# Optimization experiments

Measured on AMD Instinct MI355X. Metric: run time of the kernel, lower is better.

The kernel has to match this reference:

```python
import jax, jax.numpy as jnp
import numpy as np

B, CIN, COUT, H, W = 4, 4, 8, 256, 256
FFTH, FFTW = 2 * H - 1, 2 * W - 1  # fftsize = insize + outsize - 1 (padding=True, stride=1)


def setup_inputs() -> dict:
    key = jax.random.key(0)
    k_im, k_w, k_b = jax.random.split(key, 3)
    im = jax.random.normal(k_im, (B, CIN, H, W), dtype=jnp.float32)
    # learned frequency-domain kernel, last dim = (real, imag)
    weight = jax.random.normal(k_w, (COUT, CIN, FFTH, FFTW, 2), dtype=jnp.float32)
    bias = jax.random.normal(k_b, (COUT, 1, 1), dtype=jnp.float32)
    return {"im": im, "weight": weight, "bias": bias}


def reference(im, weight, bias):
    b, cin, h, w = im.shape
    ffth, fftw = 2 * h - 1, 2 * w - 1
    # zero-pad spatially to fftsize; imaginary part is zero (torch pads a trailing complex dim)
    im_p = jnp.pad(im, ((0, 0), (0, 0), (0, ffth - h), (0, fftw - w)))
    f_im = jnp.fft.fft2(im_p.astype(jnp.complex64))              # [B, Cin, fftH, fftW]
    wc = jax.lax.complex(weight[..., 0], weight[..., 1])         # [O, Cin, fftH, fftW]
    # broadcast complex multiply + in-channel reduction fused as a per-frequency contraction;
    # ifft is linear so summing over in-channels before ifft matches the original math
    feats = jnp.einsum('bchw,ochw->bohw', f_im, wc)              # [B, O, fftH, fftW]
    real = jnp.fft.ifft2(feats).real                             # real_feats_mode='index' -> real part
    # crop: cropsize = fftsize - insize = (H-1, W-1); left = floor/2, right = ceil/2
    cl_h, cr_h = (h - 1) // 2, h // 2
    cl_w, cr_w = (w - 1) // 2, w // 2
    real = real[:, :, cl_h:ffth - cr_h, cl_w:fftw - cr_w]        # [B, O, H, W]
    return real + bias                                           # bias [O,1,1] broadcasts
```

## Files before the change

kernel.cpp:

```cpp
#include <hip/hip_runtime.h>
#include <math.h>

#define NN 511
#define HH 256
#define BB 4
#define CINC 4
#define COUTC 8
#define CROP 127
#define INV_NN2 (1.0f / ((float)NN * (float)NN))

typedef _Float16 f16;
typedef _Float16 f16x2 __attribute__((ext_vector_type(2)));
typedef _Float16 f16x8 __attribute__((ext_vector_type(8)));
typedef float    f32x4 __attribute__((ext_vector_type(4)));

__device__ __forceinline__ void twid(int a, int b, float& c, float& s) {
    int m = (a * b) % NN;
    float phi = (float)(2.0 * M_PI / (double)NN) * (float)m;
    __sincosf(phi, &s, &c);
}

__global__ void prep_all(const float* __restrict__ im,
                         f16* __restrict__ Aa, f16* __restrict__ Bb,
                         f16* __restrict__ Bd, f16* __restrict__ Ae,
                         f16* __restrict__ imT) {
    int idx = blockIdx.x * 256 + threadIdx.x;
    if (idx < 131072) {
        int m = idx >> 8, y = idx & 255;
        float c, s;
        if (m < 256) { twid(m, y, c, s);       Aa[idx] = (f16)c;    }
        else         { twid(m - 256, y, c, s); Aa[idx] = (f16)(-s); }
    } else if (idx < 655360) {
        int i = idx - 131072;
        int n = i >> 9, k = i & 511;
        int v = n >> 1, ri = n & 1;
        float val = 0.f;
        if (v < NN) {
            int x = k & 255;
            float c, s; twid(v, x, c, s);
            if (ri == 0) val = (k < 256) ? c  : s;
            else         val = (k < 256) ? -s : c;
        }
        Bb[i] = (f16)val;
    } else if (idx < 1179648) {
        int i = idx - 655360;
        int n = i >> 10, k = i & 1023;
        int v = k >> 1, ri = k & 1;
        float val = 0.f;
        if (v < NN) {
            int x = n & 255;
            float c, s; twid(v, x + CROP, c, s);
            if (ri == 0) val = (n < 256) ? c  : s;
            else         val = (n < 256) ? -s : c;
        }
        Bd[i] = (f16)val;
    } else if (idx < 1310720) {
        int i = idx - 1179648;
        int y = i >> 9, k = i & 511;
        float c, s;
        if (k < 256) { twid(k, y + CROP, c, s);       Ae[i] = (f16)c;    }
        else         { twid(k - 256, y + CROP, c, s); Ae[i] = (f16)(-s); }
    } else if (idx < 2359296) {
        int i = idx - 1310720;
        int bc = i >> 16, r = i & 65535;
        int y = r >> 8, x = r & 255;
        imT[(size_t)bc * 65536 + x * 256 + y] = (f16)im[i];
    }
}

#define GLB_PTR(p) ((const __attribute__((address_space(1))) unsigned int*)(p))
#define LDS_PTR(p) ((__attribute__((address_space(3))) unsigned int*)(p))
__device__ __forceinline__ void gld16(const f16* g, f16* l) {
    __builtin_amdgcn_global_load_lds(GLB_PTR(g), LDS_PTR(l), 16, 0, 0);
}

#define STAGE(Abuf, Bbuf)                         \
    do {                                          \
        gld16(Ap,            (Abuf) + o8);        \
        gld16(Ap + 32 * ldA, (Abuf) + o8 + 2048); \
        gld16(Ap + 64 * ldA, (Abuf) + o8 + 4096); \
        gld16(Ap + 96 * ldA, (Abuf) + o8 + 6144); \
        gld16(Bp,            (Bbuf) + o8);        \
        gld16(Bp + 32 * ldB, (Bbuf) + o8 + 2048); \
        Ap += 64; Bp += 64;                       \
    } while (0)

#define COMPUTE(Abuf, Bbuf)                                                   \
    do {                                                                      \
        const f16* a_col = (Abuf) + (wm + col) * 64;                          \
        const f16* b_col = (Bbuf) + (wn + col) * 64;                          \
        f16x8 af[4][2], bf[2][2];                                             \
        _Pragma("unroll")                                                     \
        for (int i = 0; i < 4; ++i) {                                         \
            af[i][0] = *(const f16x8*)(a_col + i * 16 * 64 + offK0);          \
            af[i][1] = *(const f16x8*)(a_col + i * 16 * 64 + offK1);          \
        }                                                                     \
        _Pragma("unroll")                                                     \
        for (int j = 0; j < 2; ++j) {                                         \
            bf[j][0] = *(const f16x8*)(b_col + j * 16 * 64 + offK0);          \
            bf[j][1] = *(const f16x8*)(b_col + j * 16 * 64 + offK1);          \
        }                                                                     \
        _Pragma("unroll")                                                     \
        for (int kk = 0; kk < 2; ++kk)                                        \
            _Pragma("unroll")                                                 \
            for (int i = 0; i < 4; ++i)                                       \
                _Pragma("unroll")                                             \
                for (int j = 0; j < 2; ++j)                                   \
                    acc[i][j] = __builtin_amdgcn_mfma_f32_16x16x32_f16(       \
                        af[i][kk], bf[j][kk], acc[i][j], 0, 0, 0);            \
    } while (0)

#define GEMM_PREAMBLE                                                         \
    const int t    = threadIdx.x;                                             \
    const int row  = t >> 3;                                                  \
    const int slot = t & 7;                                                   \
    const int kg   = (slot ^ (row & 7)) << 3;                                 \
    const f16* Ap = A  + (size_t)(m0 + row) * ldA + kg;                       \
    const f16* Bp = Bt + (size_t)(n0 + row) * ldB + kg;                       \
    const int o8 = t * 8;                                                     \
    const int lane = t & 63, w = t >> 6;                                      \
    const int wm = (w >> 1) * 64, wn = (w & 1) * 32;                          \
    const int col = lane & 15, quad = lane >> 4;                              \
    const int aswz = col & 7;                                                 \
    const int offK0 = ((quad)     ^ aswz) << 3;                               \
    const int offK1 = ((4 + quad) ^ aswz) << 3;                               \
    f32x4 acc[4][2] = {};                                                     \
    STAGE(As0, Bs0);                                                          \
    for (int kb = 0; kb < Kt; kb += 2) {                                      \
        __syncthreads();                                                      \
        STAGE(As1, Bs1);                                                      \
        COMPUTE(As0, Bs0);                                                    \
        __syncthreads();                                                      \
        if (kb + 2 < Kt) STAGE(As0, Bs0);                                     \
        COMPUTE(As1, Bs1);                                                    \
    }

template<int EPI>
__global__ __launch_bounds__(256)
void gemm128x64(const f16* __restrict__ A, const f16* __restrict__ Bt,
                f16* __restrict__ Ch, float* __restrict__ Cf,
                const float* __restrict__ bias,
                int Kt, int ldA, int ldB, size_t sA, size_t sB) {
    __shared__ __align__(16) f16 As0[128 * 64];
    __shared__ __align__(16) f16 As1[128 * 64];
    __shared__ __align__(16) f16 Bs0[64 * 64];
    __shared__ __align__(16) f16 Bs1[64 * 64];

    const int z  = blockIdx.z;
    const int m0 = blockIdx.x * 128;
    const int n0 = blockIdx.y * 64;
    A  += (size_t)z * sA;
    Bt += (size_t)z * sB;

    GEMM_PREAMBLE

    #pragma unroll
    for (int i = 0; i < 4; ++i)
    #pragma unroll
    for (int j = 0; j < 2; ++j) {
        const int mbase = m0 + wm + i * 16 + quad * 4;
        const int ncol  = n0 + wn + j * 16 + col;
        #pragma unroll
        for (int r = 0; r < 4; ++r) {
            const int mm = mbase + r;
            const float val = acc[i][j][r];
            if constexpr (EPI == 0) {
                int u = mm & 255;
                int slotc = (mm < 256) ? ncol : 256 + ncol;
                Ch[((size_t)(u * 16 + z)) * 512 + slotc] = (f16)val;
            } else if constexpr (EPI == 2) {
                int bo = mm >> 8, u = mm & 255;
                int x     = (ncol < 256) ? ncol : ncol - 256;
                int slotc = (ncol < 256) ? u : 256 + u;
                Ch[((size_t)((bo << 8) + x)) * 512 + slotc] = (f16)val;
            } else {
                int bo = ncol >> 8, x = ncol & 255;
                Cf[((size_t)bo * 256 + mm) * 256 + x] = val + bias[bo & 7];
            }
        }
    }
}

#define LSTR 68
__global__ __launch_bounds__(256)
void gemmB_fused(const f16* __restrict__ A, const f16* __restrict__ Bt,
                 const float2* __restrict__ W, f16* __restrict__ feats) {
    __shared__ __align__(16) f16 As0[128 * 64];
    __shared__ __align__(16) f16 As1[128 * 64];
    __shared__ __align__(16) f16 Bs0[64 * 64];
    __shared__ __align__(16) f16 Bs1[64 * 64];

    const int m0 = blockIdx.x * 128;
    const int n0 = blockIdx.y * 64;
    const int Kt = 8, ldA = 512, ldB = 512;

    GEMM_PREAMBLE

    f16* Ls = As0;
    __syncthreads();
    #pragma unroll
    for (int i = 0; i < 4; ++i)
    #pragma unroll
    for (int j = 0; j < 2; ++j) {
        const int ml = wm + i * 16 + quad * 4;
        const int nl = wn + j * 16 + col;
        #pragma unroll
        for (int r = 0; r < 4; ++r)
            Ls[(ml + r) * LSTR + nl] = (f16)acc[i][j][r];
    }
    __syncthreads();

    const int du = t >> 5, dv = t & 31;
    const int u = (m0 >> 4) + du;
    const int v = (n0 >> 1) + dv;
    const int u2 = (u == 0) ? 0 : NN - u;
    const int v2 = (v == 0) ? 0 : NN - v;
    const float gu = (u == 0) ? INV_NN2 : 2.f * INV_NN2;

    float fr[16], fi[16];
    #pragma unroll
    for (int bc = 0; bc < 16; ++bc) {
        f16x2 p = *(const f16x2*)&Ls[(du * 16 + bc) * LSTR + dv * 2];
        fr[bc] = (float)p.x;
        fi[bc] = (float)p.y;
    }

    #pragma unroll
    for (int o = 0; o < COUTC; ++o) {
        float whr[CINC], whi[CINC];
        #pragma unroll
        for (int c = 0; c < CINC; ++c) {
            size_t base = (size_t)(o * CINC + c) * NN;
            float2 w1 = W[(base + u)  * NN + v];
            float2 w2 = W[(base + u2) * NN + v2];
            whr[c] = 0.5f * (w1.x + w2.x);
            whi[c] = 0.5f * (w1.y - w2.y);
        }
        #pragma unroll
        for (int b = 0; b < BB; ++b) {
            float hr = 0.f, hi = 0.f;
            #pragma unroll
            for (int c = 0; c < CINC; ++c) {
                hr += fr[b * 4 + c] * whr[c] - fi[b * 4 + c] * whi[c];
                hi += fr[b * 4 + c] * whi[c] + fi[b * 4 + c] * whr[c];
            }
            f16x2 outp; outp.x = (f16)(hr * gu); outp.y = (f16)(hi * gu);
            *(f16x2*)&feats[((size_t)((b * COUTC + o) * 256 + u)) * 1024 + v * 2] = outp;
        }
    }
}

extern "C" void kernel_launch(void* const* d_in, const int* in_sizes, int n_in,
                              void* d_out, int out_size, void* d_ws, size_t ws_size,
                              hipStream_t stream) {
    const float*  im   = (const float*)d_in[0];
    const float2* W    = (const float2*)d_in[1];
    const float*  bias = (const float*)d_in[2];
    float*        out  = (float*)d_out;

    char* ws = (char*)d_ws;
    f16* Aa    = (f16*)(ws);
    f16* Bb    = (f16*)(ws + 262144);
    f16* Bd    = (f16*)(ws + 1310720);
    f16* Ae    = (f16*)(ws + 2359296);
    f16* imT   = (f16*)(ws + 2621440);
    f16* T1    = (f16*)(ws + 4718592);
    f16* feats = (f16*)(ws + 8912896);
    f16* T2t   = (f16*)(ws + 25690112);

    prep_all<<<9216, 256, 0, stream>>>(im, Aa, Bb, Bd, Ae, imT);

    gemm128x64<0><<<dim3(4, 4, 16), 256, 0, stream>>>(Aa, imT, T1, nullptr, nullptr,
                                                      4, 256, 256, 0, 65536);
    gemmB_fused<<<dim3(32, 16), 256, 0, stream>>>(T1, Bb, W, feats);

    gemm128x64<2><<<dim3(64, 8, 1), 256, 0, stream>>>(feats, Bd, T2t, nullptr, nullptr,
                                                      16, 1024, 1024, 0, 0);
    gemm128x64<3><<<dim3(2, 128, 1), 256, 0, stream>>>(Ae, T2t, nullptr, out, bias,
                                                       8, 512, 512, 0, 0);
}
```

Baseline: 150.3 us.

## Switch GEMM tiles to 32x32x16 MFMA and coalesce image transpose writes

New measurement: 148.5 us. No clear change (-1.2%).

```diff
diff --git a/kernel.cpp b/kernel.cpp
--- a/kernel.cpp
+++ b/kernel.cpp
@@ -12,7 +12,7 @@
 typedef _Float16 f16;
 typedef _Float16 f16x2 __attribute__((ext_vector_type(2)));
 typedef _Float16 f16x8 __attribute__((ext_vector_type(8)));
-typedef float    f32x4 __attribute__((ext_vector_type(4)));
+typedef float    f32x16 __attribute__((ext_vector_type(16)));
 
 __device__ __forceinline__ void twid(int a, int b, float& c, float& s) {
     int m = (a * b) % NN;
@@ -63,8 +63,8 @@
     } else if (idx < 2359296) {
         int i = idx - 1310720;
         int bc = i >> 16, r = i & 65535;
-        int y = r >> 8, x = r & 255;
-        imT[(size_t)bc * 65536 + x * 256 + y] = (f16)im[i];
+        int x = r >> 8, y = r & 255;
+        imT[i] = (f16)im[(size_t)bc * 65536 + y * 256 + x];
     }
 }
 
@@ -87,27 +87,15 @@
 
 #define COMPUTE(Abuf, Bbuf)                                                   \
     do {                                                                      \
-        const f16* a_col = (Abuf) + (wm + col) * 64;                          \
-        const f16* b_col = (Bbuf) + (wn + col) * 64;                          \
-        f16x8 af[4][2], bf[2][2];                                             \
         _Pragma("unroll")                                                     \
-        for (int i = 0; i < 4; ++i) {                                         \
-            af[i][0] = *(const f16x8*)(a_col + i * 16 * 64 + offK0);          \
-            af[i][1] = *(const f16x8*)(a_col + i * 16 * 64 + offK1);          \
+        for (int s = 0; s < 4; ++s) {                                         \
+            const int off = (((s << 1) | kh) ^ swz) << 3;                     \
+            f16x8 a0 = *(const f16x8*)((Abuf) + (wm + ln31) * 64 + off);      \
+            f16x8 a1 = *(const f16x8*)((Abuf) + (wm + 32 + ln31) * 64 + off); \
+            f16x8 b  = *(const f16x8*)((Bbuf) + (wn + ln31) * 64 + off);      \
+            acc0 = __builtin_amdgcn_mfma_f32_32x32x16_f16(a0, b, acc0, 0, 0, 0); \
+            acc1 = __builtin_amdgcn_mfma_f32_32x32x16_f16(a1, b, acc1, 0, 0, 0); \
         }                                                                     \
-        _Pragma("unroll")                                                     \
-        for (int j = 0; j < 2; ++j) {                                         \
-            bf[j][0] = *(const f16x8*)(b_col + j * 16 * 64 + offK0);          \
-            bf[j][1] = *(const f16x8*)(b_col + j * 16 * 64 + offK1);          \
-        }                                                                     \
-        _Pragma("unroll")                                                     \
-        for (int kk = 0; kk < 2; ++kk)                                        \
-            _Pragma("unroll")                                                 \
-            for (int i = 0; i < 4; ++i)                                       \
-                _Pragma("unroll")                                             \
-                for (int j = 0; j < 2; ++j)                                   \
-                    acc[i][j] = __builtin_amdgcn_mfma_f32_16x16x32_f16(       \
-                        af[i][kk], bf[j][kk], acc[i][j], 0, 0, 0);            \
     } while (0)
 
 #define GEMM_PREAMBLE                                                         \
@@ -120,11 +108,9 @@
     const int o8 = t * 8;                                                     \
     const int lane = t & 63, w = t >> 6;                                      \
     const int wm = (w >> 1) * 64, wn = (w & 1) * 32;                          \
-    const int col = lane & 15, quad = lane >> 4;                              \
-    const int aswz = col & 7;                                                 \
-    const int offK0 = ((quad)     ^ aswz) << 3;                               \
-    const int offK1 = ((4 + quad) ^ aswz) << 3;                               \
-    f32x4 acc[4][2] = {};                                                     \
+    const int ln31 = lane & 31, kh = lane >> 5;                               \
+    const int swz = ln31 & 7;                                                 \
+    f32x16 acc0 = {}, acc1 = {};                                              \
     STAGE(As0, Bs0);                                                          \
     for (int kb = 0; kb < Kt; kb += 2) {                                      \
         __syncthreads();                                                      \
@@ -133,6 +119,18 @@
         __syncthreads();                                                      \
         if (kb + 2 < Kt) STAGE(As0, Bs0);                                     \
         COMPUTE(As1, Bs1);                                                    \
+    }
+
+#define EPILOOP(...)                                                          \
+    _Pragma("unroll")                                                         \
+    for (int ib = 0; ib < 2; ++ib) {                                          \
+        _Pragma("unroll")                                                     \
+        for (int r = 0; r < 16; ++r) {                                        \
+            const int ml   = wm + ib * 32 + (r & 3) + 8 * (r >> 2) + 4 * kh;  \
+            const int ncol = n0 + wn + ln31;                                  \
+            const float val = ib ? acc1[r] : acc0[r];                         \
+            __VA_ARGS__                                                       \
+        }                                                                     \
     }
 
 template<int EPI>
@@ -154,31 +152,24 @@
 
     GEMM_PREAMBLE
 
-    #pragma unroll
-    for (int i = 0; i < 4; ++i)
-    #pragma unroll
-    for (int j = 0; j < 2; ++j) {
-        const int mbase = m0 + wm + i * 16 + quad * 4;
-        const int ncol  = n0 + wn + j * 16 + col;
-        #pragma unroll
-        for (int r = 0; r < 4; ++r) {
-            const int mm = mbase + r;
-            const float val = acc[i][j][r];
-            if constexpr (EPI == 0) {
-                int u = mm & 255;
-                int slotc = (mm < 256) ? ncol : 256 + ncol;
-                Ch[((size_t)(u * 16 + z)) * 512 + slotc] = (f16)val;
-            } else if constexpr (EPI == 2) {
-                int bo = mm >> 8, u = mm & 255;
-                int x     = (ncol < 256) ? ncol : ncol - 256;
-                int slotc = (ncol < 256) ? u : 256 + u;
-                Ch[((size_t)((bo << 8) + x)) * 512 + slotc] = (f16)val;
-            } else {
-                int bo = ncol >> 8, x = ncol & 255;
-                Cf[((size_t)bo * 256 + mm) * 256 + x] = val + bias[bo & 7];
-            }
-        }
-    }
+    EPILOOP(
+        const int mm = m0 + ml;
+        if constexpr (EPI == 0) {
+            int u = mm & 255;
+            int slotc = (mm < 256) ? ncol : 256 + ncol;
+            Ch[((size_t)(u * 16 + z)) * 512 + slotc] = (f16)val;
+        } else if constexpr (EPI == 2) {
+            int bo = mm >> 8;
+            int u = mm & 255;
+            int x     = (ncol < 256) ? ncol : ncol - 256;
+            int slotc = (ncol < 256) ? u : 256 + u;
+            Ch[((size_t)((bo << 8) + x)) * 512 + slotc] = (f16)val;
+        } else {
+            int bo = ncol >> 8;
+            int x = ncol & 255;
+            Cf[((size_t)bo * 256 + mm) * 256 + x] = val + bias[bo & 7];
+        }
+    )
 }
 
 #define LSTR 68
@@ -198,16 +189,10 @@
 
     f16* Ls = As0;
     __syncthreads();
-    #pragma unroll
-    for (int i = 0; i < 4; ++i)
-    #pragma unroll
-    for (int j = 0; j < 2; ++j) {
-        const int ml = wm + i * 16 + quad * 4;
-        const int nl = wn + j * 16 + col;
-        #pragma unroll
-        for (int r = 0; r < 4; ++r)
-            Ls[(ml + r) * LSTR + nl] = (f16)acc[i][j][r];
-    }
+    EPILOOP(
+        const int nl = ncol - n0;
+        Ls[ml * LSTR + nl] = (f16)val;
+    )
     __syncthreads();
 
     const int du = t >> 5, dv = t & 31;
```
